# Kernel tuning notes

Measured on AMD Instinct MI355X. Metric: run time of the kernel, lower is better.

Reference implementation:

```python
import jax, jax.numpy as jnp
import numpy as np

B, L1, L2, D = 128, 256, 256, 768
NEG = -10000.0
EPS = 1e-8


def setup_inputs() -> dict:
    key = jax.random.key(0)
    k1, k2, k3, k4 = jax.random.split(key, 4)
    v1 = jax.random.normal(k1, (B, L1, D), dtype=jnp.float32)
    v2 = jax.random.normal(k2, (B, L2, D), dtype=jnp.float32)
    # masks from random valid lengths in [L//2, L]
    len1 = jax.random.randint(k3, (B,), L1 // 2, L1 + 1)
    len2 = jax.random.randint(k4, (B,), L2 // 2, L2 + 1)
    mask1 = (jnp.arange(L1)[None, :] < len1[:, None]).astype(jnp.float32)
    mask2 = (jnp.arange(L2)[None, :] < len2[:, None]).astype(jnp.float32)
    return {"v1": v1, "mask1": mask1, "v2": v2, "mask2": mask2}


def reference(v1, mask1, v2, mask2):
    # alignment matrix [B, L1, L2]
    match = jnp.einsum('bld,bmd->blm', v1, v2)
    pair_mask = (mask1[:, :, None] * mask2[:, None, :]) > 0
    match = jnp.where(pair_mask, match, NEG)
    # attention over side 1: negative max-pool over L2, scaled
    s1 = -jnp.max(match, axis=2) / 100.0            # [B, L1]
    s1 = jnp.where(mask1 > 0, s1, NEG)
    attn1 = jax.nn.softmax(s1, axis=1)
    p1 = jnp.einsum('bld,bl->bd', v1, attn1)        # [B, D]
    # attention over side 2: negative max-pool over L1, scaled
    s2 = -jnp.max(match, axis=1) / 100.0            # [B, L2]
    s2 = jnp.where(mask2 > 0, s2, NEG)
    attn2 = jax.nn.softmax(s2, axis=1)
    p2 = jnp.einsum('bmd,bm->bd', v2, attn2)        # [B, D]
    # torch.nn.functional.cosine_similarity semantics (per-vector norm clamp)
    n1 = jnp.maximum(jnp.linalg.norm(p1, axis=-1), EPS)
    n2 = jnp.maximum(jnp.linalg.norm(p2, axis=-1), EPS)
    return jnp.sum(p1 * p2, axis=-1) / (n1 * n2)
```

## Files before the change

kernel.cpp:

```cpp
#include <hip/hip_runtime.h>


#define B_   128
#define L_   256
#define D_   768
#define NEGV (-10000.0f)

typedef _Float16 f16x8 __attribute__((ext_vector_type(8)));
typedef float    f32x4 __attribute__((ext_vector_type(4)));

#define BT   128
#define BKH  64
#define NKT  (D_ / BKH)

__device__ __forceinline__ unsigned fmap(float f) {
    unsigned u = __float_as_uint(f);
    return (u & 0x80000000u) ? ~u : (u | 0x80000000u);
}
__device__ __forceinline__ float fdecode(unsigned u) {
    return __uint_as_float((u & 0x80000000u) ? (u ^ 0x80000000u) : ~u);
}
__device__ __forceinline__ float wred_max(float v) {
    #pragma unroll
    for (int o = 32; o; o >>= 1) v = fmaxf(v, __shfl_xor(v, o));
    return v;
}
__device__ __forceinline__ float wred_sum(float v) {
    #pragma unroll
    for (int o = 32; o; o >>= 1) v += __shfl_xor(v, o);
    return v;
}

__global__ __launch_bounds__(256, 2)
void k_match_max(const float* __restrict__ v1, const float* __restrict__ m1,
                 const float* __restrict__ v2, const float* __restrict__ m2,
                 unsigned* __restrict__ ru1, unsigned* __restrict__ ru2)
{
    __shared__ __align__(16) _Float16 As[BT * BKH];
    __shared__ __align__(16) _Float16 Bs[BT * BKH];
    __shared__ unsigned rU[BT], cU[BT];
    __shared__ float m1s[BT], m2s[BT];

    const int nwg = gridDim.x;
    const int cpx = nwg >> 3;
    const int wg  = (blockIdx.x & 7) * cpx + (blockIdx.x >> 3);
    const int b = wg >> 2, ti = (wg >> 1) & 1, tj = wg & 1;

    const int t = threadIdx.x;
    const int lane = t & 63, w = t >> 6;
    const int wr = w >> 1, wc = w & 1;
    const int fr = lane & 15, fg = lane >> 4;

    if (t < BT) {
        rU[t] = 0u; cU[t] = 0u;
        m1s[t] = m1[b * L_ + ti * BT + t];
        m2s[t] = m2[b * L_ + tj * BT + t];
    }

    const float* pa = v1 + ((size_t)b * L_ + ti * BT) * D_;
    const float* pb = v2 + ((size_t)b * L_ + tj * BT) * D_;

    float4 ra[4][2], rb[4][2];

    #define LOADT(kt)                                                         \
        _Pragma("unroll")                                                     \
        for (int rr = 0; rr < 4; ++rr) {                                      \
            int idx = rr * 256 + t;                 \
            int row = idx >> 3;                                               \
            int cf  = (kt) * BKH + ((idx & 7) << 3);                          \
            const float* A  = pa + (size_t)row * D_ + cf;                     \
            const float* Bp = pb + (size_t)row * D_ + cf;                     \
            ra[rr][0] = *(const float4*)A;  ra[rr][1] = *(const float4*)(A + 4);  \
            rb[rr][0] = *(const float4*)Bp; rb[rr][1] = *(const float4*)(Bp + 4); \
        }

    f32x4 acc[4][4] = {};
    LOADT(0);
    for (int kt = 0; kt < NKT; ++kt) {
        __syncthreads();
        #pragma unroll
        for (int rr = 0; rr < 4; ++rr) {
            int idx = rr * 256 + t;
            int row = idx >> 3;
            int blk = (idx & 7) ^ (row & 7);
            f16x8 ah, bh;
            #pragma unroll
            for (int q = 0; q < 4; ++q) {
                ah[q]     = (_Float16)ra[rr][0][q]; ah[4 + q] = (_Float16)ra[rr][1][q];
                bh[q]     = (_Float16)rb[rr][0][q]; bh[4 + q] = (_Float16)rb[rr][1][q];
            }
            *(f16x8*)&As[row * BKH + blk * 8] = ah;
            *(f16x8*)&Bs[row * BKH + blk * 8] = bh;
        }
        __syncthreads();
        if (kt + 1 < NKT) { LOADT(kt + 1); }
        #pragma unroll
        for (int ks = 0; ks < 2; ++ks) {
            f16x8 af[4], bf[4];
            #pragma unroll
            for (int i = 0; i < 4; ++i) {
                int r1 = wr * 64 + i * 16 + fr;
                int r2 = wc * 64 + i * 16 + fr;
                af[i] = *(const f16x8*)&As[r1 * BKH + (((ks * 4 + fg) ^ (r1 & 7)) << 3)];
                bf[i] = *(const f16x8*)&Bs[r2 * BKH + (((ks * 4 + fg) ^ (r2 & 7)) << 3)];
            }
            #pragma unroll
            for (int i = 0; i < 4; ++i)
                #pragma unroll
                for (int j = 0; j < 4; ++j)
                    acc[i][j] = __builtin_amdgcn_mfma_f32_16x16x32_f16(af[i], bf[j], acc[i][j], 0, 0, 0);
        }
    }
    #undef LOADT

    #pragma unroll
    for (int i = 0; i < 4; ++i)
        #pragma unroll
        for (int r = 0; r < 4; ++r) {
            int row = wr * 64 + i * 16 + fg * 4 + r;
            bool rv = m1s[row] > 0.f;
            float mx = NEGV;
            #pragma unroll
            for (int j = 0; j < 4; ++j) {
                int col = wc * 64 + j * 16 + fr;
                float vv = (rv && m2s[col] > 0.f) ? acc[i][j][r] : NEGV;
                mx = fmaxf(mx, vv);
            }
            atomicMax(&rU[row], fmap(mx));
        }
    #pragma unroll
    for (int j = 0; j < 4; ++j) {
        int col = wc * 64 + j * 16 + fr;
        bool cv = m2s[col] > 0.f;
        float mx = NEGV;
        #pragma unroll
        for (int i = 0; i < 4; ++i)
            #pragma unroll
            for (int r = 0; r < 4; ++r) {
                int row = wr * 64 + i * 16 + fg * 4 + r;
                float vv = (cv && m1s[row] > 0.f) ? acc[i][j][r] : NEGV;
                mx = fmaxf(mx, vv);
            }
        atomicMax(&cU[col], fmap(mx));
    }
    __syncthreads();
    if (t < BT) atomicMax(&ru1[b * L_ + ti * BT + t], rU[t]);
    else        atomicMax(&ru2[b * L_ + tj * BT + (t - BT)], cU[t - BT]);
}

__global__ __launch_bounds__(256)
void k_attn_pool(const float* __restrict__ v1, const float* __restrict__ m1,
                 const float* __restrict__ v2, const float* __restrict__ m2,
                 const unsigned* __restrict__ ru1, const unsigned* __restrict__ ru2,
                 float* __restrict__ pout)
{
    const int b = blockIdx.x, side = blockIdx.y;
    const float* v     = side ? v2 : v1;
    const float* mk    = side ? m2 : m1;
    const unsigned* ru = side ? ru2 : ru1;
    const int t = threadIdx.x, lane = t & 63, w = t >> 6;

    __shared__ float attn[L_];
    __shared__ float sred[4];

    float mkv = mk[b * L_ + t];
    float s = (mkv > 0.f) ? (-fdecode(ru[b * L_ + t]) / 100.0f) : NEGV;

    float wm = wred_max(s);
    if (lane == 0) sred[w] = wm;
    __syncthreads();
    float mx = fmaxf(fmaxf(sred[0], sred[1]), fmaxf(sred[2], sred[3]));
    float e = expf(s - mx);
    __syncthreads();
    float ws = wred_sum(e);
    if (lane == 0) sred[w] = ws;
    __syncthreads();
    float sum = sred[0] + sred[1] + sred[2] + sred[3];
    attn[t] = e / sum;
    __syncthreads();

    const float* vb = v + (size_t)b * L_ * D_;
    float p0 = 0.f, p1 = 0.f, p2 = 0.f;
    #pragma unroll 4
    for (int l = 0; l < L_; ++l) {
        float a = attn[l];
        const float* r = vb + (size_t)l * D_;
        p0 += a * r[t];
        p1 += a * r[t + 256];
        p2 += a * r[t + 512];
    }
    float* po = pout + ((size_t)b * 2 + side) * D_;
    po[t] = p0; po[t + 256] = p1; po[t + 512] = p2;
}

__global__ __launch_bounds__(256)
void k_cos(const float* __restrict__ pout, float* __restrict__ out)
{
    const int b = blockIdx.x, t = threadIdx.x, lane = t & 63, w = t >> 6;
    const float* p1 = pout + (size_t)b * 2 * D_;
    const float* p2 = p1 + D_;
    float dot = 0.f, n1 = 0.f, n2 = 0.f;
    for (int d = t; d < D_; d += 256) {
        float a = p1[d], c = p2[d];
        dot += a * c; n1 += a * a; n2 += c * c;
    }
    dot = wred_sum(dot); n1 = wred_sum(n1); n2 = wred_sum(n2);
    __shared__ float sd[4], sa[4], sc[4];
    if (lane == 0) { sd[w] = dot; sa[w] = n1; sc[w] = n2; }
    __syncthreads();
    if (t == 0) {
        float dd = sd[0] + sd[1] + sd[2] + sd[3];
        float aa = sa[0] + sa[1] + sa[2] + sa[3];
        float cc = sc[0] + sc[1] + sc[2] + sc[3];
        out[b] = dd / (fmaxf(sqrtf(aa), 1e-8f) * fmaxf(sqrtf(cc), 1e-8f));
    }
}

extern "C" void kernel_launch(void* const* d_in, const int* in_sizes, int n_in,
                              void* d_out, int out_size, void* d_ws, size_t ws_size,
                              hipStream_t stream)
{
    const float* v1 = (const float*)d_in[0];
    const float* m1 = (const float*)d_in[1];
    const float* v2 = (const float*)d_in[2];
    const float* m2 = (const float*)d_in[3];
    float* out = (float*)d_out;

    unsigned* ru1 = (unsigned*)d_ws;
    unsigned* ru2 = ru1 + (size_t)B_ * L_;
    float*    pout = (float*)(ru2 + (size_t)B_ * L_);

    hipMemsetAsync(d_ws, 0, 2 * (size_t)B_ * L_ * sizeof(unsigned), stream);

    k_match_max<<<dim3((L_ / BT) * (L_ / BT) * B_), 256, 0, stream>>>(v1, m1, v2, m2, ru1, ru2);

    dim3 g2(B_, 2);
    k_attn_pool<<<g2, 256, 0, stream>>>(v1, m1, v2, m2, ru1, ru2, pout);

    k_cos<<<B_, 256, 0, stream>>>(pout, out);
}
```

Baseline: 82.97 us.

## Use 512-thread GEMM blocks and split attention pooling across D chunks

```diff
diff --git a/kernel.cpp b/kernel.cpp
--- a/kernel.cpp
+++ b/kernel.cpp
@@ -31,7 +31,7 @@
     return v;
 }
 
-__global__ __launch_bounds__(256, 2)
+__global__ __launch_bounds__(512, 4)
 void k_match_max(const float* __restrict__ v1, const float* __restrict__ m1,
                  const float* __restrict__ v2, const float* __restrict__ m2,
                  unsigned* __restrict__ ru1, unsigned* __restrict__ ru2)
@@ -41,9 +41,8 @@
     __shared__ unsigned rU[BT], cU[BT];
     __shared__ float m1s[BT], m2s[BT];
 
-    const int nwg = gridDim.x;
-    const int cpx = nwg >> 3;
-    const int wg  = (blockIdx.x & 7) * cpx + (blockIdx.x >> 3);
+    const int bid = blockIdx.x;
+    const int wg  = (bid & 7) * 64 + (bid >> 3);
     const int b = wg >> 2, ti = (wg >> 1) & 1, tj = wg & 1;
 
     const int t = threadIdx.x;
@@ -60,52 +59,56 @@
     const float* pa = v1 + ((size_t)b * L_ + ti * BT) * D_;
     const float* pb = v2 + ((size_t)b * L_ + tj * BT) * D_;
 
-    float4 ra[4][2], rb[4][2];
-
-    #define LOADT(kt)                                                         \
-        _Pragma("unroll")                                                     \
-        for (int rr = 0; rr < 4; ++rr) {                                      \
-            int idx = rr * 256 + t;                 \
-            int row = idx >> 3;                                               \
-            int cf  = (kt) * BKH + ((idx & 7) << 3);                          \
-            const float* A  = pa + (size_t)row * D_ + cf;                     \
-            const float* Bp = pb + (size_t)row * D_ + cf;                     \
-            ra[rr][0] = *(const float4*)A;  ra[rr][1] = *(const float4*)(A + 4);  \
-            rb[rr][0] = *(const float4*)Bp; rb[rr][1] = *(const float4*)(Bp + 4); \
-        }
-
-    f32x4 acc[4][4] = {};
+    float4 ra[2][2], rb[2][2];
+
+    #define LOADT(kt)                                                          \
+        _Pragma("unroll")                                                      \
+        for (int g = 0; g < 2; ++g) {                                          \
+            int idx = g * 512 + t;                   \
+            int row = idx >> 3;                                                \
+            int cf  = (kt) * BKH + ((idx & 7) << 3);                           \
+            const float* A  = pa + (size_t)row * D_ + cf;                      \
+            const float* Bp = pb + (size_t)row * D_ + cf;                      \
+            ra[g][0] = *(const float4*)A;  ra[g][1] = *(const float4*)(A + 4); \
+            rb[g][0] = *(const float4*)Bp; rb[g][1] = *(const float4*)(Bp + 4);\
+        }
+
+    f32x4 acc[2][4] = {};
     LOADT(0);
     for (int kt = 0; kt < NKT; ++kt) {
         __syncthreads();
         #pragma unroll
-        for (int rr = 0; rr < 4; ++rr) {
-            int idx = rr * 256 + t;
+        for (int g = 0; g < 2; ++g) {
+            int idx = g * 512 + t;
             int row = idx >> 3;
             int blk = (idx & 7) ^ (row & 7);
             f16x8 ah, bh;
             #pragma unroll
             for (int q = 0; q < 4; ++q) {
-                ah[q]     = (_Float16)ra[rr][0][q]; ah[4 + q] = (_Float16)ra[rr][1][q];
-                bh[q]     = (_Float16)rb[rr][0][q]; bh[4 + q] = (_Float16)rb[rr][1][q];
+                ah[q] = (_Float16)ra[g][0][q]; ah[4 + q] = (_Float16)ra[g][1][q];
+                bh[q] = (_Float16)rb[g][0][q]; bh[4 + q] = (_Float16)rb[g][1][q];
             }
             *(f16x8*)&As[row * BKH + blk * 8] = ah;
             *(f16x8*)&Bs[row * BKH + blk * 8] = bh;
         }
         __syncthreads();
         if (kt + 1 < NKT) { LOADT(kt + 1); }
+        __builtin_amdgcn_sched_barrier(0);
         #pragma unroll
         for (int ks = 0; ks < 2; ++ks) {
-            f16x8 af[4], bf[4];
-            #pragma unroll
-            for (int i = 0; i < 4; ++i) {
-                int r1 = wr * 64 + i * 16 + fr;
-                int r2 = wc * 64 + i * 16 + fr;
+            f16x8 af[2], bf[4];
+            #pragma unroll
+            for (int i = 0; i < 2; ++i) {
+                int r1 = wr * 32 + i * 16 + fr;
                 af[i] = *(const f16x8*)&As[r1 * BKH + (((ks * 4 + fg) ^ (r1 & 7)) << 3)];
-                bf[i] = *(const f16x8*)&Bs[r2 * BKH + (((ks * 4 + fg) ^ (r2 & 7)) << 3)];
-            }
-            #pragma unroll
-            for (int i = 0; i < 4; ++i)
+            }
+            #pragma unroll
+            for (int j = 0; j < 4; ++j) {
+                int r2 = wc * 64 + j * 16 + fr;
+                bf[j] = *(const f16x8*)&Bs[r2 * BKH + (((ks * 4 + fg) ^ (r2 & 7)) << 3)];
+            }
+            #pragma unroll
+            for (int i = 0; i < 2; ++i)
                 #pragma unroll
                 for (int j = 0; j < 4; ++j)
                     acc[i][j] = __builtin_amdgcn_mfma_f32_16x16x32_f16(af[i], bf[j], acc[i][j], 0, 0, 0);
@@ -114,10 +117,10 @@
     #undef LOADT
 
     #pragma unroll
-    for (int i = 0; i < 4; ++i)
+    for (int i = 0; i < 2; ++i)
         #pragma unroll
         for (int r = 0; r < 4; ++r) {
-            int row = wr * 64 + i * 16 + fg * 4 + r;
+            int row = wr * 32 + i * 16 + fg * 4 + r;
             bool rv = m1s[row] > 0.f;
             float mx = NEGV;
             #pragma unroll
@@ -134,18 +137,18 @@
         bool cv = m2s[col] > 0.f;
         float mx = NEGV;
         #pragma unroll
-        for (int i = 0; i < 4; ++i)
+        for (int i = 0; i < 2; ++i)
             #pragma unroll
             for (int r = 0; r < 4; ++r) {
-                int row = wr * 64 + i * 16 + fg * 4 + r;
+                int row = wr * 32 + i * 16 + fg * 4 + r;
                 float vv = (cv && m1s[row] > 0.f) ? acc[i][j][r] : NEGV;
                 mx = fmaxf(mx, vv);
             }
         atomicMax(&cU[col], fmap(mx));
     }
     __syncthreads();
-    if (t < BT) atomicMax(&ru1[b * L_ + ti * BT + t], rU[t]);
-    else        atomicMax(&ru2[b * L_ + tj * BT + (t - BT)], cU[t - BT]);
+    if (t < BT)            atomicMax(&ru1[b * L_ + ti * BT + t], rU[t]);
+    else if (t < 2 * BT)   atomicMax(&ru2[b * L_ + tj * BT + (t - BT)], cU[t - BT]);
 }
 
 __global__ __launch_bounds__(256)
@@ -154,7 +157,10 @@
                  const unsigned* __restrict__ ru1, const unsigned* __restrict__ ru2,
                  float* __restrict__ pout)
 {
-    const int b = blockIdx.x, side = blockIdx.y;
+    const int lin = (int)blockIdx.x;
+    const int swz = (lin & 7) * 96 + (lin >> 3);
+    const int b = swz / 6, rem = swz % 6, side = rem / 3, chunk = rem % 3;
+
     const float* v     = side ? v2 : v1;
     const float* mk    = side ? m2 : m1;
     const unsigned* ru = side ? ru2 : ru1;
@@ -179,18 +185,12 @@
     attn[t] = e / sum;
     __syncthreads();
 
-    const float* vb = v + (size_t)b * L_ * D_;
-    float p0 = 0.f, p1 = 0.f, p2 = 0.f;
-    #pragma unroll 4
-    for (int l = 0; l < L_; ++l) {
-        float a = attn[l];
-        const float* r = vb + (size_t)l * D_;
-        p0 += a * r[t];
-        p1 += a * r[t + 256];
-        p2 += a * r[t + 512];
-    }
-    float* po = pout + ((size_t)b * 2 + side) * D_;
-    po[t] = p0; po[t + 256] = p1; po[t + 512] = p2;
+    const int d = chunk * 256 + t;
+    const float* vb = v + (size_t)b * L_ * D_ + d;
+    float p = 0.f;
+    #pragma unroll 8
+    for (int l = 0; l < L_; ++l) p += attn[l] * vb[(size_t)l * D_];
+    pout[((size_t)b * 2 + side) * D_ + d] = p;
 }
 
 __global__ __launch_bounds__(256)
@@ -232,10 +232,9 @@
 
     hipMemsetAsync(d_ws, 0, 2 * (size_t)B_ * L_ * sizeof(unsigned), stream);
 
-    k_match_max<<<dim3((L_ / BT) * (L_ / BT) * B_), 256, 0, stream>>>(v1, m1, v2, m2, ru1, ru2);
-
-    dim3 g2(B_, 2);
-    k_attn_pool<<<g2, 256, 0, stream>>>(v1, m1, v2, m2, ru1, ru2, pout);
+    k_match_max<<<dim3((L_ / BT) * (L_ / BT) * B_), 512, 0, stream>>>(v1, m1, v2, m2, ru1, ru2);
+
+    k_attn_pool<<<dim3(B_ * 2 * 3), 256, 0, stream>>>(v1, m1, v2, m2, ru1, ru2, pout);
 
     k_cos<<<B_, 256, 0, stream>>>(pout, out);
 }
```

Measured after the change: 80.28 us. 3.2% less time.
